# Performance work log

Measured on AMD Instinct MI355X. Metric: run time of the kernel, lower is better.

## Reference

```python
import jax, jax.numpy as jnp
import numpy as np

EMBED = 1024
HEADS = 16
HEAD_DIM = EMBED // HEADS


def setup_inputs() -> dict:
    key = jax.random.key(0)
    ks = jax.random.split(key, 8)
    N, S = 4, 2048
    values = jax.random.normal(ks[0], (N, S, EMBED), dtype=jnp.float32)
    queries = jax.random.normal(ks[1], (N, S, EMBED), dtype=jnp.float32)
    keys = jax.random.normal(ks[2], (N, S, EMBED), dtype=jnp.float32)
    mask = jax.random.randint(ks[3], (N, 1, S, S), 0, 2, dtype=jnp.int32)
    sc = 1.0 / np.sqrt(HEAD_DIM)
    Wv = jax.random.normal(ks[4], (HEAD_DIM, HEAD_DIM), dtype=jnp.float32) * sc
    Wk = jax.random.normal(ks[5], (HEAD_DIM, HEAD_DIM), dtype=jnp.float32) * sc
    Wq = jax.random.normal(ks[6], (HEAD_DIM, HEAD_DIM), dtype=jnp.float32) * sc
    Wo = jax.random.normal(ks[7], (EMBED, EMBED), dtype=jnp.float32) * (1.0 / np.sqrt(EMBED))
    bo = jnp.zeros((EMBED,), dtype=jnp.float32)
    return {"values": values, "queries": queries, "keys": keys, "mask": mask,
            "Wv": Wv, "Wk": Wk, "Wq": Wq, "Wo": Wo, "bo": bo}


def reference(values, queries, keys, mask, Wv, Wk, Wq, Wo, bo):
    N, S, _ = queries.shape
    # split heads: (N, len, H, D)
    v = values.reshape(N, -1, HEADS, HEAD_DIM)
    k = keys.reshape(N, -1, HEADS, HEAD_DIM)
    q = queries.reshape(N, -1, HEADS, HEAD_DIM)
    # per-head linear projections (nn.Linear: y = x @ W.T, no bias)
    v = jnp.einsum('nlhd,ed->nlhe', v, Wv)
    k = jnp.einsum('nlhd,ed->nlhe', k, Wk)
    q = jnp.einsum('nlhd,ed->nlhe', q, Wq)
    # energy: (N, H, q_len, k_len)
    energy = jnp.einsum('nqhd,nkhd->nhqk', q, k)
    energy = jnp.where(mask == 0, jnp.float32(-1e20), energy)
    # non-standard scale: sqrt(embed_size), applied after masking
    attn = jax.nn.softmax(energy / jnp.sqrt(jnp.float32(EMBED)), axis=3)
    out = jnp.einsum('nhql,nlhd->nqhd', attn, v).reshape(N, S, EMBED)
    return out @ Wo.T + bo
```

## Files before the change

kernel.cpp:

```cpp
#include <hip/hip_runtime.h>
#include <hip/hip_bf16.h>

#define NBATCH 4
#define SEQ    2048
#define EMBED  1024
#define HEADS  16
#define HD     64

typedef __attribute__((ext_vector_type(8))) short bf16x8;
typedef __attribute__((ext_vector_type(4))) float f32x4;
typedef __attribute__((ext_vector_type(16))) float f32x16;

__device__ __forceinline__ short f2bf(float f) {
  union { float f; unsigned u; } v; v.f = f;
  unsigned r = v.u + 0x7fffu + ((v.u >> 16) & 1u);
  return (short)(r >> 16);
}

__device__ __forceinline__ unsigned pkbf(float a, float b) {
#if __has_builtin(__builtin_amdgcn_cvt_pk_bf16_f32)
  typedef __attribute__((ext_vector_type(2))) __bf16 bf16x2_t;
  bf16x2_t r = __builtin_amdgcn_cvt_pk_bf16_f32(a, b);
  union { bf16x2_t v; unsigned u; } cv; cv.v = r; return cv.u;
#else
  return (unsigned)(unsigned short)f2bf(a) | ((unsigned)(unsigned short)f2bf(b) << 16);
#endif
}

typedef __attribute__((address_space(1))) const void gas_void;
typedef __attribute__((address_space(3))) void las_void;
__device__ __forceinline__ void glds16(const void* g, void* l) {
  __builtin_amdgcn_global_load_lds((gas_void*)g, (las_void*)l, 16, 0, 0);
}

__device__ __forceinline__ bf16x8 mk8(unsigned a, unsigned b, unsigned c, unsigned d) {
  union { unsigned u[4]; bf16x8 v; } t;
  t.u[0] = a; t.u[1] = b; t.u[2] = c; t.u[3] = d; return t.v;
}

__device__ __forceinline__ void pl32swap(unsigned &a, unsigned &b) {
  asm volatile("v_permlane32_swap_b32 %0, %1" : "+v"(a), "+v"(b));
}

#define MFMA32(A, B, C) __builtin_amdgcn_mfma_f32_32x32x16_bf16((A), (B), (C), 0, 0, 0)

#define C2 0.04508422f

__global__ __launch_bounds__(256) void cvt_all(
    const float* __restrict__ Wo, const float* __restrict__ Wq,
    const float* __restrict__ Wk, const float* __restrict__ Wv,
    short* __restrict__ dWo, short* __restrict__ dWq,
    short* __restrict__ dWk, short* __restrict__ dWv)
{
  int e = (blockIdx.x * 256 + threadIdx.x) * 4;
  const float* src; short* dst; int off; float sc = 1.0f;
  if (e < EMBED * EMBED) { src = Wo; dst = dWo; off = e; }
  else {
    int j = e - EMBED * EMBED;
    if      (j < 4096)  { src = Wq; dst = dWq; off = j; sc = C2; }
    else if (j < 8192)  { src = Wk; dst = dWk; off = j - 4096; }
    else if (j < 12288) { src = Wv; dst = dWv; off = j - 8192; }
    else return;
  }
  float4 v = *(const float4*)(src + off);
  ushort4 p;
  p.x = (unsigned short)f2bf(v.x * sc);
  p.y = (unsigned short)f2bf(v.y * sc);
  p.z = (unsigned short)f2bf(v.z * sc);
  p.w = (unsigned short)f2bf(v.w * sc);
  *(ushort4*)(dst + off) = p;
}

__global__ __launch_bounds__(256) void mask_pack(const int* __restrict__ mask,
                                                 unsigned long long* __restrict__ bits) {
  long long t = (long long)blockIdx.x * 256 + threadIdx.x;
  int lane = threadIdx.x & 63;
  int m = mask[t];
  unsigned long long b = __ballot(m != 0);
  if (lane == 0) bits[t >> 6] = b;
}

__global__ __launch_bounds__(256) void proj_kernel(
    const float* __restrict__ srcQ, const float* __restrict__ srcK, const float* __restrict__ srcV,
    const short* __restrict__ WbQ, const short* __restrict__ WbK, const short* __restrict__ WbV,
    short* __restrict__ Qp, short* __restrict__ Kp, short* __restrict__ Vt)
{
  int rt = blockIdx.x;
  int h  = blockIdx.y;
  int mz = blockIdx.z;
  const float* src = (mz == 0) ? srcQ : ((mz == 1) ? srcK : srcV);
  const short* Wb  = (mz == 0) ? WbQ : ((mz == 1) ? WbK : WbV);

  __shared__ __align__(16) short At[64][72];

  int tid = threadIdx.x;
  int r0 = rt * 64;
  for (int idx = tid; idx < 64 * 16; idx += 256) {
    int row = idx >> 4;
    int c4  = idx & 15;
    float4 v = *(const float4*)(src + (long long)(r0 + row) * EMBED + h * HD + c4 * 4);
    uint2 pk2;
    pk2.x = pkbf(v.x, v.y);
    pk2.y = pkbf(v.z, v.w);
    *(uint2*)&At[row][c4 * 4] = pk2;
  }
  __syncthreads();

  int lane = tid & 63, w = tid >> 6, quad = lane >> 4, l15 = lane & 15;

  bf16x8 af0 = *(const bf16x8*)&At[w * 16 + l15][quad * 8];
  bf16x8 af1 = *(const bf16x8*)&At[w * 16 + l15][32 + quad * 8];

  f32x4 acc[4];
  for (int cg = 0; cg < 4; cg++) {
    acc[cg] = (f32x4){0.f, 0.f, 0.f, 0.f};
    bf16x8 b0 = *(const bf16x8*)(Wb + (cg * 16 + l15) * 64 + quad * 8);
    bf16x8 b1 = *(const bf16x8*)(Wb + (cg * 16 + l15) * 64 + 32 + quad * 8);
    acc[cg] = __builtin_amdgcn_mfma_f32_16x16x32_bf16(af0, b0, acc[cg], 0, 0, 0);
    acc[cg] = __builtin_amdgcn_mfma_f32_16x16x32_bf16(af1, b1, acc[cg], 0, 0, 0);
  }

  int rloc = w * 16 + quad * 4;
  if (mz < 2) {
    short* dst = (mz == 0) ? Qp : Kp;
    for (int cg = 0; cg < 4; cg++) {
      for (int reg = 0; reg < 4; reg++) {
        int r = r0 + rloc + reg;
        int n = r >> 11, s = r & 2047;
        dst[((long long)(n * HEADS + h) * SEQ + s) * HD + cg * 16 + l15] = f2bf(acc[cg][reg]);
      }
    }
  } else {
    int r = r0 + rloc;
    int n = r >> 11, s = r & 2047;
    for (int cg = 0; cg < 4; cg++) {
      int d = cg * 16 + l15;
      uint2 pk2;
      pk2.x = pkbf(acc[cg][0], acc[cg][1]);
      pk2.y = pkbf(acc[cg][2], acc[cg][3]);
      *(uint2*)(Vt + ((long long)(n * HEADS + h) * HD + d) * SEQ + s) = pk2;
    }
  }
}

#define SOFTMAX_KK(SV, MW, PAV0, PAV1) do {                                       \
    unsigned n0 = ((MW) >> sh4) & 0xFu;                                           \
    unsigned n1 = ((MW) >> (sh4 + 8)) & 0xFu;                                     \
    unsigned n2 = ((MW) >> (sh4 + 16)) & 0xFu;                                    \
    unsigned n3 = ((MW) >> (sh4 + 24)) & 0xFu;                                    \
    float p0  = __builtin_amdgcn_exp2f(SV[0]);   p0  = (n0 & 1u) ? p0  : 0.f;     \
    float p1  = __builtin_amdgcn_exp2f(SV[1]);   p1  = (n0 & 2u) ? p1  : 0.f;     \
    float p2  = __builtin_amdgcn_exp2f(SV[2]);   p2  = (n0 & 4u) ? p2  : 0.f;     \
    float p3  = __builtin_amdgcn_exp2f(SV[3]);   p3  = (n0 & 8u) ? p3  : 0.f;     \
    float p4  = __builtin_amdgcn_exp2f(SV[4]);   p4  = (n1 & 1u) ? p4  : 0.f;     \
    float p5  = __builtin_amdgcn_exp2f(SV[5]);   p5  = (n1 & 2u) ? p5  : 0.f;     \
    float p6  = __builtin_amdgcn_exp2f(SV[6]);   p6  = (n1 & 4u) ? p6  : 0.f;     \
    float p7  = __builtin_amdgcn_exp2f(SV[7]);   p7  = (n1 & 8u) ? p7  : 0.f;     \
    float p8  = __builtin_amdgcn_exp2f(SV[8]);   p8  = (n2 & 1u) ? p8  : 0.f;     \
    float p9  = __builtin_amdgcn_exp2f(SV[9]);   p9  = (n2 & 2u) ? p9  : 0.f;     \
    float p10 = __builtin_amdgcn_exp2f(SV[10]);  p10 = (n2 & 4u) ? p10 : 0.f;     \
    float p11 = __builtin_amdgcn_exp2f(SV[11]);  p11 = (n2 & 8u) ? p11 : 0.f;     \
    float p12 = __builtin_amdgcn_exp2f(SV[12]);  p12 = (n3 & 1u) ? p12 : 0.f;     \
    float p13 = __builtin_amdgcn_exp2f(SV[13]);  p13 = (n3 & 2u) ? p13 : 0.f;     \
    float p14 = __builtin_amdgcn_exp2f(SV[14]);  p14 = (n3 & 4u) ? p14 : 0.f;     \
    float p15 = __builtin_amdgcn_exp2f(SV[15]);  p15 = (n3 & 8u) ? p15 : 0.f;     \
    lsum += (((p0 + p1) + (p2 + p3)) + ((p4 + p5) + (p6 + p7)))                   \
          + (((p8 + p9) + (p10 + p11)) + ((p12 + p13) + (p14 + p15)));            \
    unsigned u0 = pkbf(p0, p1),   u1 = pkbf(p2, p3);                              \
    unsigned u2 = pkbf(p4, p5),   u3 = pkbf(p6, p7);                              \
    unsigned u4 = pkbf(p8, p9),   u5 = pkbf(p10, p11);                            \
    unsigned u6 = pkbf(p12, p13), u7 = pkbf(p14, p15);                            \
    pl32swap(u0, u2); pl32swap(u1, u3);                                           \
    pl32swap(u4, u6); pl32swap(u5, u7);                                           \
    PAV0 = mk8(u0, u1, u2, u3);                                                   \
    PAV1 = mk8(u4, u5, u6, u7);                                                   \
  } while (0)

#define ATTN_ITER(BUF, KT) do {                                                   \
    __syncthreads();                                                              \
    if ((KT) < 31) {                                                              \
      const char* ks_ = Kb + ((KT) + 1) * 8192 + kgo;                             \
      const char* vs_ = Vb + ((KT) + 1) * 128 + vgo;                              \
      char* kd_ = ldsK + (((BUF) ^ 1) * 8192) + klo;                              \
      char* vd_ = ldsV + (((BUF) ^ 1) * 8192) + klo;                              \
      glds16(ks_,          kd_);                                                  \
      glds16(ks_ + 4096,   kd_ + 4096);                                           \
      glds16(vs_,          vd_);                                                  \
      glds16(vs_ + 131072, vd_ + 4096);                                           \
      mnxt = mptr[(KT) + 1];                                                      \
    }                                                                             \
    unsigned mlo = (unsigned)mcur, mhiw = (unsigned)(mcur >> 32);                 \
    const char* KB_ = ldsK + (BUF) * 8192;                                        \
    const char* VB_ = ldsV + (BUF) * 8192;                                        \
    bf16x8 pa0, pa1, pa2, pa3;                                                    \
    {                                                                             \
      f32x16 s = {};                                                              \
      __builtin_amdgcn_s_setprio(1);                                              \
      s = MFMA32(*(const bf16x8*)(KB_ + a4_0), qf0, s);                           \
      s = MFMA32(*(const bf16x8*)(KB_ + a4_1), qf1, s);                           \
      s = MFMA32(*(const bf16x8*)(KB_ + a4_2), qf2, s);                           \
      s = MFMA32(*(const bf16x8*)(KB_ + a4_3), qf3, s);                           \
      __builtin_amdgcn_s_setprio(0);                                              \
      SOFTMAX_KK(s, mlo, pa0, pa1);                                               \
    }                                                                             \
    {                                                                             \
      f32x16 s = {};                                                              \
      __builtin_amdgcn_s_setprio(1);                                              \
      s = MFMA32(*(const bf16x8*)(KB_ + 4096 + a4_0), qf0, s);                    \
      s = MFMA32(*(const bf16x8*)(KB_ + 4096 + a4_1), qf1, s);                    \
      s = MFMA32(*(const bf16x8*)(KB_ + 4096 + a4_2), qf2, s);                    \
      s = MFMA32(*(const bf16x8*)(KB_ + 4096 + a4_3), qf3, s);                    \
      __builtin_amdgcn_s_setprio(0);                                              \
      SOFTMAX_KK(s, mhiw, pa2, pa3);                                              \
    }                                                                             \
    __builtin_amdgcn_s_setprio(1);                                                \
    O0 = MFMA32(*(const bf16x8*)(VB_ + a4_0),        pa0, O0);                    \
    O1 = MFMA32(*(const bf16x8*)(VB_ + 4096 + a4_0), pa0, O1);                    \
    O0 = MFMA32(*(const bf16x8*)(VB_ + a4_1),        pa1, O0);                    \
    O1 = MFMA32(*(const bf16x8*)(VB_ + 4096 + a4_1), pa1, O1);                    \
    O0 = MFMA32(*(const bf16x8*)(VB_ + a4_2),        pa2, O0);                    \
    O1 = MFMA32(*(const bf16x8*)(VB_ + 4096 + a4_2), pa2, O1);                    \
    O0 = MFMA32(*(const bf16x8*)(VB_ + a4_3),        pa3, O0);                    \
    O1 = MFMA32(*(const bf16x8*)(VB_ + 4096 + a4_3), pa3, O1);                    \
    __builtin_amdgcn_s_setprio(0);                                                \
    mcur = mnxt;                                                                  \
  } while (0)

__global__ __launch_bounds__(256, 3) void attn_kernel(
    const short* __restrict__ Qp, const short* __restrict__ Kp, const short* __restrict__ Vt,
    const unsigned long long* __restrict__ mbits, short* __restrict__ AO)
{
  int qt = blockIdx.x, h = blockIdx.y, nb = blockIdx.z;
  int q0 = qt * 128;

  __shared__ __align__(16) char ldsK[2 * 8192];
  __shared__ __align__(16) char ldsV[2 * 8192];

  int tid = threadIdx.x, lane = tid & 63, w = tid >> 6;
  int l31 = lane & 31, hi5 = lane >> 5;
  int g8 = lane & 7, r8 = lane >> 3;
  int pp = lane & 7;
  unsigned sh4 = (unsigned)(hi5 * 4);

  long long nh = (long long)(nb * HEADS + h);
  const char* Kb = (const char*)(Kp + nh * SEQ * HD);
  const char* Vb = (const char*)(Vt + nh * HD * SEQ);

  int kgo = (w * 8 + r8) * 128 + ((g8 ^ r8) << 4);
  int vgo = (w * 8 + r8) * 4096 + ((g8 ^ r8) << 4);
  int klo = w * 1024;

  int a4_0 = l31 * 128 + ((((0 | hi5) ^ pp)) << 4);
  int a4_1 = l31 * 128 + ((((2 | hi5) ^ pp)) << 4);
  int a4_2 = l31 * 128 + ((((4 | hi5) ^ pp)) << 4);
  int a4_3 = l31 * 128 + ((((6 | hi5) ^ pp)) << 4);

  int qrow = q0 + w * 32 + l31;
  const short* Qb = Qp + (nh * SEQ + qrow) * HD + hi5 * 8;
  bf16x8 qf0 = *(const bf16x8*)(Qb);
  bf16x8 qf1 = *(const bf16x8*)(Qb + 16);
  bf16x8 qf2 = *(const bf16x8*)(Qb + 32);
  bf16x8 qf3 = *(const bf16x8*)(Qb + 48);

  const unsigned long long* mptr = mbits + ((long long)nb * SEQ + qrow) * 32;

  f32x16 O0 = {}, O1 = {};
  float lsum = 0.f;

  glds16(Kb + kgo,          ldsK + klo);
  glds16(Kb + 4096 + kgo,   ldsK + 4096 + klo);
  glds16(Vb + vgo,          ldsV + klo);
  glds16(Vb + vgo + 131072, ldsV + 4096 + klo);
  unsigned long long mcur = mptr[0], mnxt = 0;

  for (int it = 0; it < 16; it++) {
    ATTN_ITER(0, it * 2);
    ATTN_ITER(1, it * 2 + 1);
  }

  lsum += __shfl_xor(lsum, 32);
  float inv = 1.f / lsum;

  short* aoRow = AO + ((long long)nb * SEQ + qrow) * EMBED + h * HD + hi5 * 4;
#pragma unroll
  for (int j = 0; j < 4; j++) {
    uint2 pk;
    pk.x = pkbf(O0[4 * j] * inv, O0[4 * j + 1] * inv);
    pk.y = pkbf(O0[4 * j + 2] * inv, O0[4 * j + 3] * inv);
    *(uint2*)(aoRow + j * 8) = pk;
    pk.x = pkbf(O1[4 * j] * inv, O1[4 * j + 1] * inv);
    pk.y = pkbf(O1[4 * j + 2] * inv, O1[4 * j + 3] * inv);
    *(uint2*)(aoRow + 32 + j * 8) = pk;
  }
}

__global__ __launch_bounds__(256) void outproj_kernel(
    const short* __restrict__ AO, const short* __restrict__ Wob,
    const float* __restrict__ bo, float* __restrict__ out)
{
  int rt = blockIdx.x, ct = blockIdx.y;
  __shared__ __align__(16) short AtL[128 * 64];
  __shared__ __align__(16) short BtL[128 * 64];

  int tid = threadIdx.x, lane = tid & 63, w = tid >> 6, quad = lane >> 4, l15 = lane & 15;
  int g8 = lane & 7, r8 = lane >> 3;
  int swz = g8 ^ r8;
  int s3 = l15 & 7;
  int o0 = (quad ^ s3) * 16;
  int o1 = ((quad + 4) ^ s3) * 16;

  int r0 = rt * 128, c0 = ct * 128;
  int wr = (w >> 1) * 64, wc = (w & 1) * 64;

  const char* Abase = (const char*)AO  + (long long)(r0 + w * 8 + r8) * 2048 + swz * 16;
  const char* Bbase = (const char*)Wob + (long long)(c0 + w * 8 + r8) * 2048 + swz * 16;
  unsigned lbase = (unsigned)(w * 8) * 128;

  f32x4 acc[4][4];
#pragma unroll
  for (int mi = 0; mi < 4; mi++)
#pragma unroll
    for (int ni = 0; ni < 4; ni++) acc[mi][ni] = (f32x4){0.f, 0.f, 0.f, 0.f};

  for (int kc = 0; kc < 16; kc++) {
    __syncthreads();
#pragma unroll
    for (int i = 0; i < 4; i++) {
      glds16(Abase + (long long)i * 32 * 2048 + kc * 128, (char*)AtL + lbase + i * 32 * 128);
      glds16(Bbase + (long long)i * 32 * 2048 + kc * 128, (char*)BtL + lbase + i * 32 * 128);
    }
    __syncthreads();

    const char* AB = (const char*)AtL;
    const char* BB = (const char*)BtL;
    bf16x8 af[4][2], bf[4][2];
#pragma unroll
    for (int mi = 0; mi < 4; mi++) {
      int r = wr + mi * 16 + l15;
      af[mi][0] = *(const bf16x8*)(AB + r * 128 + o0);
      af[mi][1] = *(const bf16x8*)(AB + r * 128 + o1);
    }
#pragma unroll
    for (int ni = 0; ni < 4; ni++) {
      int r = wc + ni * 16 + l15;
      bf[ni][0] = *(const bf16x8*)(BB + r * 128 + o0);
      bf[ni][1] = *(const bf16x8*)(BB + r * 128 + o1);
    }
#pragma unroll
    for (int mi = 0; mi < 4; mi++)
#pragma unroll
      for (int ni = 0; ni < 4; ni++) {
        acc[mi][ni] = __builtin_amdgcn_mfma_f32_16x16x32_bf16(af[mi][0], bf[ni][0], acc[mi][ni], 0, 0, 0);
        acc[mi][ni] = __builtin_amdgcn_mfma_f32_16x16x32_bf16(af[mi][1], bf[ni][1], acc[mi][ni], 0, 0, 0);
      }
  }

#pragma unroll
  for (int ni = 0; ni < 4; ni++) {
    float b = bo[c0 + wc + ni * 16 + l15];
#pragma unroll
    for (int mi = 0; mi < 4; mi++)
#pragma unroll
      for (int reg = 0; reg < 4; reg++) {
        int r = r0 + wr + mi * 16 + quad * 4 + reg;
        out[(long long)r * EMBED + c0 + wc + ni * 16 + l15] = acc[mi][ni][reg] + b;
      }
  }
}

extern "C" void kernel_launch(void* const* d_in, const int* in_sizes, int n_in,
                              void* d_out, int out_size, void* d_ws, size_t ws_size,
                              hipStream_t stream) {
  const float* values  = (const float*)d_in[0];
  const float* queries = (const float*)d_in[1];
  const float* keys    = (const float*)d_in[2];
  const int*   mask    = (const int*)d_in[3];
  const float* Wv = (const float*)d_in[4];
  const float* Wk = (const float*)d_in[5];
  const float* Wq = (const float*)d_in[6];
  const float* Wo = (const float*)d_in[7];
  const float* bo = (const float*)d_in[8];
  float* out = (float*)d_out;

  char* ws = (char*)d_ws;
  size_t off = 0;
  const size_t PROJ_BYTES = (size_t)NBATCH * HEADS * SEQ * HD * 2;
  short* Qp = (short*)(ws + off); off += PROJ_BYTES;
  short* Kp = (short*)(ws + off); off += PROJ_BYTES;
  short* Vt = (short*)(ws + off); off += PROJ_BYTES;
  short* AO = (short*)(ws + off); off += PROJ_BYTES;
  unsigned long long* mbits = (unsigned long long*)(ws + off);
  off += (size_t)NBATCH * SEQ * (SEQ / 64) * 8;
  short* Wob = (short*)(ws + off); off += (size_t)EMBED * EMBED * 2;
  short* WbQ = (short*)(ws + off); off += HD * HD * 2;
  short* WbK = (short*)(ws + off); off += HD * HD * 2;
  short* WbV = (short*)(ws + off); off += HD * HD * 2;

  cvt_all<<<dim3((EMBED * EMBED + 3 * HD * HD) / 4 / 256), dim3(256), 0, stream>>>(
      Wo, Wq, Wk, Wv, Wob, WbQ, WbK, WbV);

  mask_pack<<<dim3((NBATCH * SEQ * SEQ) / 256), dim3(256), 0, stream>>>(mask, mbits);

  proj_kernel<<<dim3((NBATCH * SEQ) / 64, HEADS, 3), dim3(256), 0, stream>>>(
      queries, keys, values, WbQ, WbK, WbV, Qp, Kp, Vt);

  attn_kernel<<<dim3(SEQ / 128, HEADS, NBATCH), dim3(256), 0, stream>>>(Qp, Kp, Vt, mbits, AO);

  outproj_kernel<<<dim3((NBATCH * SEQ) / 128, EMBED / 128), dim3(256), 0, stream>>>(AO, Wob, bo, out);
}
```

Before: 378.0 us.

## Stage projection outputs through LDS, remap attention grid, widen outproj to 512 threads

The projection kernel now writes its bf16 results into shared memory and then emits them as coalesced 32-byte row stores, instead of scattered 2-byte or 8-byte global writes. V is transposed inside LDS. The attention launch becomes a 1D grid whose block index is remapped so that 8 consecutive blocks share a head-batch group, which may improve L2 locality for K/V. The output projection uses 512 threads (8 waves, 32x64 tiles per wave) for more waves per block and fewer per-wave registers. The cost is an extra LDS round trip and barriers in the projection kernel.

```diff
diff --git a/kernel.cpp b/kernel.cpp
--- a/kernel.cpp
+++ b/kernel.cpp
@@ -121,26 +121,36 @@
   }
 
   int rloc = w * 16 + quad * 4;
+  __syncthreads();
   if (mz < 2) {
-    short* dst = (mz == 0) ? Qp : Kp;
-    for (int cg = 0; cg < 4; cg++) {
-      for (int reg = 0; reg < 4; reg++) {
-        int r = r0 + rloc + reg;
-        int n = r >> 11, s = r & 2047;
-        dst[((long long)(n * HEADS + h) * SEQ + s) * HD + cg * 16 + l15] = f2bf(acc[cg][reg]);
-      }
-    }
+#pragma unroll
+    for (int cg = 0; cg < 4; cg++)
+#pragma unroll
+      for (int reg = 0; reg < 4; reg++)
+        At[rloc + reg][cg * 16 + l15] = f2bf(acc[cg][reg]);
   } else {
-    int r = r0 + rloc;
-    int n = r >> 11, s = r & 2047;
-    for (int cg = 0; cg < 4; cg++) {
-      int d = cg * 16 + l15;
-      uint2 pk2;
-      pk2.x = pkbf(acc[cg][0], acc[cg][1]);
-      pk2.y = pkbf(acc[cg][2], acc[cg][3]);
-      *(uint2*)(Vt + ((long long)(n * HEADS + h) * HD + d) * SEQ + s) = pk2;
-    }
-  }
+#pragma unroll
+    for (int cg = 0; cg < 4; cg++)
+#pragma unroll
+      for (int reg = 0; reg < 4; reg++)
+        At[cg * 16 + l15][rloc + reg] = f2bf(acc[cg][reg]);
+  }
+  __syncthreads();
+
+  short* dst = (mz == 0) ? Qp : ((mz == 1) ? Kp : Vt);
+  int row2 = tid >> 2, ch = tid & 3;
+  const uint4* lp = (const uint4*)&At[row2][ch * 16];
+  uint4 v0 = lp[0], v1 = lp[1];
+  char* g;
+  if (mz < 2) {
+    int r = r0 + row2; int n = r >> 11, s = r & 2047;
+    g = (char*)(dst + ((long long)(n * HEADS + h) * SEQ + s) * HD) + ch * 32;
+  } else {
+    int n = r0 >> 11, s0 = r0 & 2047;
+    g = (char*)(dst + ((long long)(n * HEADS + h) * HD + row2) * SEQ + s0) + ch * 32;
+  }
+  *(uint4*)g = v0;
+  *(uint4*)(g + 16) = v1;
 }
 
 #define SOFTMAX_KK(SV, MW, PAV0, PAV1) do {                                       \
@@ -230,7 +240,11 @@
     const short* __restrict__ Qp, const short* __restrict__ Kp, const short* __restrict__ Vt,
     const unsigned long long* __restrict__ mbits, short* __restrict__ AO)
 {
-  int qt = blockIdx.x, h = blockIdx.y, nb = blockIdx.z;
+  int L  = blockIdx.x;
+  int qt = (L >> 3) & 15;
+  int p_ = ((L >> 7) << 3) | (L & 7);
+  int h  = p_ & 15;
+  int nb = p_ >> 4;
   int q0 = qt * 128;
 
   __shared__ __align__(16) char ldsK[2 * 8192];
@@ -294,7 +308,7 @@
   }
 }
 
-__global__ __launch_bounds__(256) void outproj_kernel(
+__global__ __launch_bounds__(512) void outproj_kernel(
     const short* __restrict__ AO, const short* __restrict__ Wob,
     const float* __restrict__ bo, float* __restrict__ out)
 {
@@ -303,39 +317,38 @@
   __shared__ __align__(16) short BtL[128 * 64];
 
   int tid = threadIdx.x, lane = tid & 63, w = tid >> 6, quad = lane >> 4, l15 = lane & 15;
-  int g8 = lane & 7, r8 = lane >> 3;
-  int swz = g8 ^ r8;
+  int r8b = tid >> 3, g8 = tid & 7;
+  int swz = g8 ^ (r8b & 7);
   int s3 = l15 & 7;
   int o0 = (quad ^ s3) * 16;
   int o1 = ((quad + 4) ^ s3) * 16;
 
   int r0 = rt * 128, c0 = ct * 128;
-  int wr = (w >> 1) * 64, wc = (w & 1) * 64;
-
-  const char* Abase = (const char*)AO  + (long long)(r0 + w * 8 + r8) * 2048 + swz * 16;
-  const char* Bbase = (const char*)Wob + (long long)(c0 + w * 8 + r8) * 2048 + swz * 16;
-  unsigned lbase = (unsigned)(w * 8) * 128;
-
-  f32x4 acc[4][4];
-#pragma unroll
-  for (int mi = 0; mi < 4; mi++)
+  int wr = (w >> 1) * 32, wc = (w & 1) * 64;
+
+  const char* Abase = (const char*)AO  + (long long)(r0 + r8b) * 2048 + swz * 16;
+  const char* Bbase = (const char*)Wob + (long long)(c0 + r8b) * 2048 + swz * 16;
+  unsigned lbase = (unsigned)tid * 16;
+
+  f32x4 acc[2][4];
+#pragma unroll
+  for (int mi = 0; mi < 2; mi++)
 #pragma unroll
     for (int ni = 0; ni < 4; ni++) acc[mi][ni] = (f32x4){0.f, 0.f, 0.f, 0.f};
 
   for (int kc = 0; kc < 16; kc++) {
     __syncthreads();
-#pragma unroll
-    for (int i = 0; i < 4; i++) {
-      glds16(Abase + (long long)i * 32 * 2048 + kc * 128, (char*)AtL + lbase + i * 32 * 128);
-      glds16(Bbase + (long long)i * 32 * 2048 + kc * 128, (char*)BtL + lbase + i * 32 * 128);
-    }
+    glds16(Abase + kc * 128,                 (char*)AtL + lbase);
+    glds16(Abase + 64LL * 2048 + kc * 128,   (char*)AtL + lbase + 8192);
+    glds16(Bbase + kc * 128,                 (char*)BtL + lbase);
+    glds16(Bbase + 64LL * 2048 + kc * 128,   (char*)BtL + lbase + 8192);
     __syncthreads();
 
     const char* AB = (const char*)AtL;
     const char* BB = (const char*)BtL;
-    bf16x8 af[4][2], bf[4][2];
-#pragma unroll
-    for (int mi = 0; mi < 4; mi++) {
+    bf16x8 af[2][2];
+#pragma unroll
+    for (int mi = 0; mi < 2; mi++) {
       int r = wr + mi * 16 + l15;
       af[mi][0] = *(const bf16x8*)(AB + r * 128 + o0);
       af[mi][1] = *(const bf16x8*)(AB + r * 128 + o1);
@@ -343,23 +356,21 @@
 #pragma unroll
     for (int ni = 0; ni < 4; ni++) {
       int r = wc + ni * 16 + l15;
-      bf[ni][0] = *(const bf16x8*)(BB + r * 128 + o0);
-      bf[ni][1] = *(const bf16x8*)(BB + r * 128 + o1);
+      bf16x8 b0 = *(const bf16x8*)(BB + r * 128 + o0);
+      bf16x8 b1 = *(const bf16x8*)(BB + r * 128 + o1);
+#pragma unroll
+      for (int mi = 0; mi < 2; mi++) {
+        acc[mi][ni] = __builtin_amdgcn_mfma_f32_16x16x32_bf16(af[mi][0], b0, acc[mi][ni], 0, 0, 0);
+        acc[mi][ni] = __builtin_amdgcn_mfma_f32_16x16x32_bf16(af[mi][1], b1, acc[mi][ni], 0, 0, 0);
+      }
     }
-#pragma unroll
-    for (int mi = 0; mi < 4; mi++)
-#pragma unroll
-      for (int ni = 0; ni < 4; ni++) {
-        acc[mi][ni] = __builtin_amdgcn_mfma_f32_16x16x32_bf16(af[mi][0], bf[ni][0], acc[mi][ni], 0, 0, 0);
-        acc[mi][ni] = __builtin_amdgcn_mfma_f32_16x16x32_bf16(af[mi][1], bf[ni][1], acc[mi][ni], 0, 0, 0);
-      }
   }
 
 #pragma unroll
   for (int ni = 0; ni < 4; ni++) {
     float b = bo[c0 + wc + ni * 16 + l15];
 #pragma unroll
-    for (int mi = 0; mi < 4; mi++)
+    for (int mi = 0; mi < 2; mi++)
 #pragma unroll
       for (int reg = 0; reg < 4; reg++) {
         int r = r0 + wr + mi * 16 + quad * 4 + reg;
@@ -404,7 +415,7 @@
   proj_kernel<<<dim3((NBATCH * SEQ) / 64, HEADS, 3), dim3(256), 0, stream>>>(
       queries, keys, values, WbQ, WbK, WbV, Qp, Kp, Vt);
 
-  attn_kernel<<<dim3(SEQ / 128, HEADS, NBATCH), dim3(256), 0, stream>>>(Qp, Kp, Vt, mbits, AO);
-
-  outproj_kernel<<<dim3((NBATCH * SEQ) / 128, EMBED / 128), dim3(256), 0, stream>>>(AO, Wob, bo, out);
-}
+  attn_kernel<<<dim3(SEQ / 128 * HEADS * NBATCH), dim3(256), 0, stream>>>(Qp, Kp, Vt, mbits, AO);
+
+  outproj_kernel<<<dim3((NBATCH * SEQ) / 128, EMBED / 128), dim3(512), 0, stream>>>(AO, Wob, bo, out);
+}
```

New measurement: 367.7 us. -2.7%, faster.
